# Performance work log

Measured on AMD Instinct MI355X. Metric: run time of the kernel, lower is better.

Reference implementation:

```python
import jax, jax.numpy as jnp
import numpy as np

N = 100_000   # nodes
E = 1_600_000 # edges per edge type
DIN = 128     # input_dim
DH = 128      # prot_hidden_dim
L = 3         # prot_num_layers
EPS = 1e-5


def setup_inputs() -> dict:
    key = jax.random.key(0)
    ks = jax.random.split(key, 8)
    s = 1.0 / np.sqrt(DH)
    return {
        "x": jax.random.normal(ks[0], (N, DIN), jnp.float32),
        "src": jax.random.randint(ks[1], (3, E), 0, N, jnp.int32),
        "dst": jax.random.randint(ks[2], (3, E), 0, N, jnp.int32),
        "gc_W0": jax.random.normal(ks[3], (3, DIN, DH), jnp.float32) * s,
        "gc_b0": jnp.zeros((3, DH), jnp.float32),
        "gc_W": jax.random.normal(ks[4], (L - 1, 3, DH, DH), jnp.float32) * s,
        "gc_b": jnp.zeros((L - 1, 3, DH), jnp.float32),
        "fc_W": jax.random.normal(ks[5], (L, DH, DH), jnp.float32) * s,
        "fc_b": jnp.zeros((L, DH), jnp.float32),
        "bn_gamma": jnp.ones((L, DH), jnp.float32),
        "bn_beta": jnp.zeros((L, DH), jnp.float32),
    }


def _graph_conv(x, src, dst, W, b):
    # DGL GraphConv, norm='both': D_in^{-1/2} A D_out^{-1/2} X W + b
    ones = jnp.ones(src.shape[0], x.dtype)
    deg_out = jnp.clip(jax.ops.segment_sum(ones, src, num_segments=N), 1.0)
    deg_in = jnp.clip(jax.ops.segment_sum(ones, dst, num_segments=N), 1.0)
    # apply weight first (same math; keeps gathered message width = DH)
    h = (x * jax.lax.rsqrt(deg_out)[:, None]) @ W  # [N, DH]
    agg = jax.ops.segment_sum(h[src], dst, num_segments=N)  # gather + scatter-add
    return agg * jax.lax.rsqrt(deg_in)[:, None] + b


def _batchnorm(x, gamma, beta):
    # training-mode BatchNorm1d: biased batch statistics
    mu = jnp.mean(x, axis=0)
    var = jnp.mean(jnp.square(x - mu), axis=0)
    return (x - mu) * jax.lax.rsqrt(var + EPS) * gamma + beta


def reference(x, src, dst, gc_W0, gc_b0, gc_W, gc_b, fc_W, fc_b, bn_gamma, bn_beta):
    h = x
    for l in range(L):
        W = gc_W0 if l == 0 else gc_W[l - 1]
        b = gc_b0 if l == 0 else gc_b[l - 1]
        # HeteroGraphConv with aggregate='sum' over 3 edge types
        out = _graph_conv(h, src[0], dst[0], W[0], b[0])
        for e in range(1, 3):
            out = out + _graph_conv(h, src[e], dst[e], W[e], b[e])
        # FC -> ReLU -> BatchNorm (dropout = identity in eval mode)
        h = _batchnorm(jax.nn.relu(out @ fc_W[l] + fc_b[l]), bn_gamma[l], bn_beta[l])
    return h
```

## Files before the change

kernel.cpp:

```cpp
#include <hip/hip_runtime.h>


#define EPSV 1e-5f
#define CH 4096
#define MAXNB 512

typedef _Float16 h2v __attribute__((ext_vector_type(2)));
typedef _Float16 f16x8 __attribute__((ext_vector_type(8)));
typedef __attribute__((ext_vector_type(4))) float f4v;

__global__ void coarse_hist(const int* __restrict__ src, const int* __restrict__ dst,
                            int* __restrict__ chd, int* __restrict__ chs,
                            int E, int NB) {
    __shared__ int hd[MAXNB], hs[MAXNB];
    int t = blockIdx.y;
    for (int i = threadIdx.x; i < MAXNB; i += 256) { hd[i] = 0; hs[i] = 0; }
    __syncthreads();
    int base = blockIdx.x * CH;
    int end = base + CH < E ? base + CH : E;
    const int* sp = src + (size_t)t * E;
    const int* dp = dst + (size_t)t * E;
    for (int i = base + threadIdx.x; i < end; i += 256) {
        atomicAdd(&hd[dp[i] >> 8], 1);
        atomicAdd(&hs[sp[i] >> 8], 1);
    }
    __syncthreads();
    for (int b = threadIdx.x; b < NB; b += 256) {
        if (hd[b]) atomicAdd(&chd[t * NB + b], hd[b]);
        if (hs[b]) atomicAdd(&chs[t * NB + b], hs[b]);
    }
}

__global__ void scan_off(const int* __restrict__ chd, const int* __restrict__ chs,
                         int* __restrict__ offd, int* __restrict__ offs,
                         int* __restrict__ gcd, int* __restrict__ gcs,
                         int* __restrict__ rowptr, int NB, int N, int E) {
    __shared__ int s[MAXNB];
    int tid = threadIdx.x;
    for (int a = 0; a < 6; ++a) {
        const int* h = (a < 3) ? chd + a * NB : chs + (a - 3) * NB;
        int* off = (a < 3) ? offd + a * (NB + 1) : offs + (a - 3) * (NB + 1);
        int* gc = (a < 3) ? gcd + a * NB : gcs + (a - 3) * NB;
        s[tid] = (tid < NB) ? h[tid] : 0;
        __syncthreads();
        for (int o = 1; o < MAXNB; o <<= 1) {
            int v = (tid >= o) ? s[tid - o] : 0;
            __syncthreads();
            s[tid] += v;
            __syncthreads();
        }
        if (tid < NB) {
            off[tid + 1] = s[tid];
            if (tid == 0) off[0] = 0;
        }
        __syncthreads();
        if (tid < NB) gc[tid] = off[tid];
        __syncthreads();
    }
    if (tid < 3) rowptr[tid * (N + 1) + N] = E;
}

__launch_bounds__(256)
__global__ void scatter_coarse(const int* __restrict__ src, const int* __restrict__ dst,
                               int* __restrict__ gcd, int* __restrict__ gcs,
                               int* __restrict__ dbuf, unsigned char* __restrict__ sbuf,
                               int E, int NB) {
    __shared__ int hd[MAXNB], hs[MAXNB];
    __shared__ int lod[MAXNB], los[MAXNB];
    __shared__ int bd[MAXNB], bs[MAXNB];
    __shared__ int rbi[CH];
    __shared__ unsigned char rbs[CH];
    const int tid = threadIdx.x;
    const int t = blockIdx.y;
    const int base = blockIdx.x * CH;
    const int end = base + CH < E ? base + CH : E;
    const int cnt = end - base;
    const int* sp = src + (size_t)t * E;
    const int* dp = dst + (size_t)t * E;

    for (int i = tid; i < MAXNB; i += 256) { hd[i] = 0; hs[i] = 0; }
    __syncthreads();
    for (int i = base + tid; i < end; i += 256) {
        atomicAdd(&hd[dp[i] >> 8], 1);
        atomicAdd(&hs[sp[i] >> 8], 1);
    }
    __syncthreads();
    for (int b = tid; b < NB; b += 256) {
        bd[b] = hd[b] ? atomicAdd(&gcd[t * NB + b], hd[b]) : 0;
        bs[b] = hs[b] ? atomicAdd(&gcs[t * NB + b], hs[b]) : 0;
    }
    lod[tid] = hd[tid]; lod[tid + 256] = hd[tid + 256];
    los[tid] = hs[tid]; los[tid + 256] = hs[tid + 256];
    __syncthreads();
    for (int o = 1; o < MAXNB; o <<= 1) {
        int a0 = lod[tid], a1 = lod[tid + 256];
        int b0 = los[tid], b1 = los[tid + 256];
        int p0 = (tid >= o) ? lod[tid - o] : 0;
        int p1 = lod[tid + 256 - o];
        int q0 = (tid >= o) ? los[tid - o] : 0;
        int q1 = los[tid + 256 - o];
        __syncthreads();
        lod[tid] = a0 + p0; lod[tid + 256] = a1 + p1;
        los[tid] = b0 + q0; los[tid + 256] = b1 + q1;
        __syncthreads();
    }
    hd[tid] = lod[tid] - hd[tid]; hd[tid + 256] = lod[tid + 256] - hd[tid + 256];
    hs[tid] = los[tid] - hs[tid]; hs[tid + 256] = los[tid + 256] - hs[tid + 256];
    __syncthreads();
    for (int i = base + tid; i < end; i += 256) {
        int sv = sp[i], dv = dp[i];
        int lp = atomicAdd(&hd[dv >> 8], 1);
        rbi[lp] = (sv << 8) | (dv & 255);
        int ls = atomicAdd(&hs[sv >> 8], 1);
        rbs[ls] = (unsigned char)(sv & 255);
    }
    __syncthreads();
    for (int i = tid; i < cnt; i += 256) {
        int lo = 0, hi = NB - 1;
        while (lo < hi) { int mid = (lo + hi) >> 1; if (lod[mid] > i) hi = mid; else lo = mid + 1; }
        int excl = lo ? lod[lo - 1] : 0;
        dbuf[(size_t)t * E + bd[lo] + (i - excl)] = rbi[i];
    }
    for (int i = tid; i < cnt; i += 256) {
        int lo = 0, hi = NB - 1;
        while (lo < hi) { int mid = (lo + hi) >> 1; if (los[mid] > i) hi = mid; else lo = mid + 1; }
        int excl = lo ? los[lo - 1] : 0;
        sbuf[(size_t)t * E + bs[lo] + (i - excl)] = rbs[i];
    }
}

__global__ void fine_src(const unsigned char* __restrict__ sbuf, const int* __restrict__ offs,
                         float* __restrict__ dro, int E, int N, int NB) {
    __shared__ int h[256];
    int b = blockIdx.x, t = blockIdx.y;
    int tid = threadIdx.x;
    h[tid] = 0;
    __syncthreads();
    int beg = offs[t * (NB + 1) + b], end = offs[t * (NB + 1) + b + 1];
    const unsigned char* sp = sbuf + (size_t)t * E;
    for (int i = beg + tid; i < end; i += 256) atomicAdd(&h[sp[i]], 1);
    __syncthreads();
    int node = b * 256 + tid;
    if (node < N) {
        int dg = h[tid] < 1 ? 1 : h[tid];
        dro[(size_t)t * N + node] = rsqrtf((float)dg);
    }
}

#define FDCAP 6656
__global__ void fine_dst(const int* __restrict__ dbuf, const int* __restrict__ offd,
                         const float* __restrict__ dro, int* __restrict__ erec,
                         int* __restrict__ rowptr, float* __restrict__ dri,
                         int E, int N, int NB) {
    __shared__ int h[256], sc[256], cur[256];
    __shared__ int rb[FDCAP];
    int b = blockIdx.x, t = blockIdx.y;
    int tid = threadIdx.x;
    h[tid] = 0;
    __syncthreads();
    int beg = offd[t * (NB + 1) + b], end = offd[t * (NB + 1) + b + 1];
    int cnt = end - beg;
    const int* dp = dbuf + (size_t)t * E;
    const float* drt = dro + (size_t)t * N;
    for (int i = beg + tid; i < end; i += 256) atomicAdd(&h[dp[i] & 255], 1);
    __syncthreads();
    sc[tid] = h[tid];
    __syncthreads();
    for (int o = 1; o < 256; o <<= 1) {
        int v = (tid >= o) ? sc[tid - o] : 0;
        __syncthreads();
        sc[tid] += v;
        __syncthreads();
    }
    int excl = sc[tid] - h[tid];
    cur[tid] = excl;
    int node = b * 256 + tid;
    if (node < N) {
        rowptr[t * (N + 1) + node] = beg + excl;
        int dg = h[tid] < 1 ? 1 : h[tid];
        dri[(size_t)t * N + node] = rsqrtf((float)dg);
    }
    __syncthreads();
    if (cnt <= FDCAP) {
        for (int i = beg + tid; i < end; i += 256) {
            int v = dp[i];
            int p = atomicAdd(&cur[v & 255], 1);
            rb[p] = v >> 8;
        }
        __syncthreads();
        for (int i = tid; i < cnt; i += 256) {
            int sv = rb[i];
            int wq = (int)(drt[sv] * 4095.0f + 0.5f);
            erec[(size_t)t * E + beg + i] = sv | (wq << 20);
        }
    } else {
        for (int i = beg + tid; i < end; i += 256) {
            int v = dp[i];
            int sv = v >> 8;
            int wq = (int)(drt[sv] * 4095.0f + 0.5f);
            int p = beg + atomicAdd(&cur[v & 255], 1);
            erec[(size_t)t * E + p] = sv | (wq << 20);
        }
    }
}

__device__ __forceinline__ h2v ash2(unsigned u) {
    union { unsigned u; h2v h; } c;
    c.u = u;
    return c.h;
}
__device__ __forceinline__ unsigned packh2(float lo, float hi) {
    union { h2v h; unsigned u; } c;
    c.h = (h2v){(_Float16)lo, (_Float16)hi};
    return c.u;
}
__device__ __forceinline__ unsigned short f16b(float f) {
    union { _Float16 h; unsigned short s; } c;
    c.h = (_Float16)f;
    return c.s;
}

__global__ void cvt_f16(const float* __restrict__ h, unsigned short* __restrict__ h2,
                        int total8) {
    int i = blockIdx.x * 256 + threadIdx.x;
    if (i >= total8) return;
    const float4* hp = (const float4*)h + (size_t)i * 2;
    float4 v0 = hp[0], v1 = hp[1];
    uint4 o;
    o.x = packh2(v0.x, v0.y);
    o.y = packh2(v0.z, v0.w);
    o.z = packh2(v1.x, v1.y);
    o.w = packh2(v1.z, v1.w);
    ((uint4*)h2)[i] = o;
}

__global__ void pack_w(const float* __restrict__ gcW0, const float* __restrict__ gcW,
                       const float* __restrict__ fcW, unsigned short* __restrict__ Wg,
                       unsigned short* __restrict__ Wf) {
    int mat = blockIdx.x;
    const float* srcp;
    unsigned short* dstp;
    if (mat < 9) {
        int l = mat / 3, e = mat % 3;
        srcp = (l == 0) ? gcW0 + (size_t)e * 16384
                        : gcW + ((size_t)(l - 1) * 3 + e) * 16384;
        dstp = Wg + (size_t)mat * 16384;
    } else {
        srcp = fcW + (size_t)(mat - 9) * 16384;
        dstp = Wf + (size_t)(mat - 9) * 16384;
    }
    for (int p = threadIdx.x; p < 16384; p += 256) {
        int j = p & 7;
        int ln = (p >> 3) & 63;
        int nt = (p >> 9) & 7;
        int ks = p >> 12;
        int k = ks * 32 + (ln >> 4) * 8 + j;
        int n = nt * 16 + (ln & 15);
        dstp[p] = f16b(srcp[k * 128 + n]);
    }
}

template <int AFF>
__launch_bounds__(256)
__global__ void agg_kernel(const unsigned short* __restrict__ h2, const int* __restrict__ rowptrB,
                           const int* __restrict__ erecB, const float* __restrict__ driB,
                           const float* __restrict__ bnsum, const float* __restrict__ gamma,
                           const float* __restrict__ beta, float invn,
                           unsigned short* __restrict__ zB, int N, int E) {
    __shared__ float lss[256];
    if (AFF) {
        int tid = threadIdx.x;
        if (tid < 128) {
            float mean = bnsum[tid] * invn;
            float var = bnsum[128 + tid] * invn - mean * mean;
            float sc = gamma[tid] * rsqrtf(var + EPSV);
            lss[tid] = sc;
            lss[128 + tid] = beta[tid] - mean * sc;
        }
        __syncthreads();
    }
    const int e = blockIdx.y;
    const int* rowptr = rowptrB + e * (N + 1);
    const int* erec = erecB + (size_t)e * E;
    const float* dri = driB + (size_t)e * N;
    unsigned short* z = zB + (size_t)e * N * 128;

    int idx = blockIdx.x * 256 + threadIdx.x;
    int node = idx >> 4;
    int lq = idx & 15;
    if (node >= N) return;
    int beg = rowptr[node], end = rowptr[node + 1];
    const uint4* hp = (const uint4*)h2 + lq;
    h2v ac0 = (h2v)0, ac1 = (h2v)0, ac2 = (h2v)0, ac3 = (h2v)0;
    float wacc = 0.f;
    const float IW = 1.0f / 4095.0f;

    int j = beg;
    for (; j + 8 <= end; j += 8) {
        int r[8];
#pragma unroll
        for (int q = 0; q < 8; ++q) r[q] = erec[j + q];
        uint4 u[8];
#pragma unroll
        for (int q = 0; q < 8; ++q) u[q] = hp[(size_t)(r[q] & 0xFFFFF) * 16];
#pragma unroll
        for (int q = 0; q < 8; ++q) {
            float wf = (float)((unsigned)r[q] >> 20) * IW;
            if (AFF) wacc += wf;
            _Float16 wh = (_Float16)wf;
            h2v wp = (h2v){wh, wh};
            ac0 = ash2(u[q].x) * wp + ac0;
            ac1 = ash2(u[q].y) * wp + ac1;
            ac2 = ash2(u[q].z) * wp + ac2;
            ac3 = ash2(u[q].w) * wp + ac3;
        }
    }
    for (; j + 4 <= end; j += 4) {
        int r[4];
#pragma unroll
        for (int q = 0; q < 4; ++q) r[q] = erec[j + q];
        uint4 u[4];
#pragma unroll
        for (int q = 0; q < 4; ++q) u[q] = hp[(size_t)(r[q] & 0xFFFFF) * 16];
#pragma unroll
        for (int q = 0; q < 4; ++q) {
            float wf = (float)((unsigned)r[q] >> 20) * IW;
            if (AFF) wacc += wf;
            _Float16 wh = (_Float16)wf;
            h2v wp = (h2v){wh, wh};
            ac0 = ash2(u[q].x) * wp + ac0;
            ac1 = ash2(u[q].y) * wp + ac1;
            ac2 = ash2(u[q].z) * wp + ac2;
            ac3 = ash2(u[q].w) * wp + ac3;
        }
    }
    for (; j < end; ++j) {
        int r0 = erec[j];
        float wf = (float)((unsigned)r0 >> 20) * IW;
        if (AFF) wacc += wf;
        _Float16 wh = (_Float16)wf;
        h2v wp = (h2v){wh, wh};
        uint4 u0 = hp[(size_t)(r0 & 0xFFFFF) * 16];
        ac0 = ash2(u0.x) * wp + ac0;
        ac1 = ash2(u0.y) * wp + ac1;
        ac2 = ash2(u0.z) * wp + ac2;
        ac3 = ash2(u0.w) * wp + ac3;
    }
    float a0 = (float)ac0[0], a1 = (float)ac0[1];
    float a2 = (float)ac1[0], a3 = (float)ac1[1];
    float a4 = (float)ac2[0], a5 = (float)ac2[1];
    float a6 = (float)ac3[0], a7 = (float)ac3[1];
    float scl = dri[node];
    if (AFF) {
        const float* ap = &lss[lq * 8];
        const float* bp = &lss[128 + lq * 8];
        a0 = ap[0] * a0 + bp[0] * wacc;
        a1 = ap[1] * a1 + bp[1] * wacc;
        a2 = ap[2] * a2 + bp[2] * wacc;
        a3 = ap[3] * a3 + bp[3] * wacc;
        a4 = ap[4] * a4 + bp[4] * wacc;
        a5 = ap[5] * a5 + bp[5] * wacc;
        a6 = ap[6] * a6 + bp[6] * wacc;
        a7 = ap[7] * a7 + bp[7] * wacc;
    }
    uint4 o;
    o.x = packh2(a0 * scl, a1 * scl);
    o.y = packh2(a2 * scl, a3 * scl);
    o.z = packh2(a4 * scl, a5 * scl);
    o.w = packh2(a6 * scl, a7 * scl);
    ((uint4*)z)[(size_t)node * 16 + lq] = o;
}

template <int MODE>
__launch_bounds__(512)
__global__ void mfma_layer(const unsigned short* __restrict__ zB,
                           const unsigned short* __restrict__ Wgp,
                           const float* __restrict__ b3,
                           const unsigned short* __restrict__ Wfp,
                           const float* __restrict__ fcb,
                           unsigned short* __restrict__ outb, float* __restrict__ outf,
                           float* __restrict__ bnsum, int M) {
    __shared__ unsigned short T[128 * 128];
    __shared__ float red[256];
    const int tid = threadIdx.x;
    const int l = tid & 63;
    const int wv = tid >> 6;
    const int wm = wv >> 1;
    const int wn = wv & 1;
    const int m0 = blockIdx.x * 128;
    const int lr = l & 15;
    const int lk = (l >> 4) * 8;

    int rowb[2];
#pragma unroll
    for (int mt = 0; mt < 2; ++mt) {
        int r = m0 + wm * 32 + mt * 16 + lr;
        rowb[mt] = (r < M) ? r : (M - 1);
    }

    {
        f4v acc[2][4];
#pragma unroll
        for (int i = 0; i < 2; ++i)
#pragma unroll
            for (int j = 0; j < 4; ++j) acc[i][j] = (f4v){0.f, 0.f, 0.f, 0.f};
#pragma unroll
        for (int e = 0; e < 3; ++e) {
            const unsigned short* zp = zB + (size_t)e * M * 128;
            const unsigned short* wp = Wgp + (size_t)e * 16384;
#pragma unroll
            for (int ks = 0; ks < 4; ++ks) {
                f16x8 a[2], b[4];
#pragma unroll
                for (int mt = 0; mt < 2; ++mt)
                    a[mt] = *(const f16x8*)(zp + (size_t)rowb[mt] * 128 + ks * 32 + lk);
#pragma unroll
                for (int nt = 0; nt < 4; ++nt)
                    b[nt] = *(const f16x8*)(wp + ks * 4096 + (wn * 4 + nt) * 512 + l * 8);
#pragma unroll
                for (int mt = 0; mt < 2; ++mt)
#pragma unroll
                    for (int nt = 0; nt < 4; ++nt)
                        acc[mt][nt] = __builtin_amdgcn_mfma_f32_16x16x32_f16(
                            a[mt], b[nt], acc[mt][nt], 0, 0, 0);
            }
        }
        float bs[4];
        int col[4];
#pragma unroll
        for (int nt = 0; nt < 4; ++nt) {
            col[nt] = wn * 64 + nt * 16 + lr;
            bs[nt] = b3[col[nt]] + b3[128 + col[nt]] + b3[256 + col[nt]];
        }
#pragma unroll
        for (int mt = 0; mt < 2; ++mt) {
#pragma unroll
            for (int r = 0; r < 4; ++r) {
                int rl = wm * 32 + mt * 16 + (l >> 4) * 4 + r;
#pragma unroll
                for (int nt = 0; nt < 4; ++nt) {
                    int c = col[nt];
                    int chunk = (c >> 3) ^ (rl & 15);
                    T[rl * 128 + chunk * 8 + (c & 7)] = f16b(acc[mt][nt][r] + bs[nt]);
                }
            }
        }
    }
    __syncthreads();

    f4v acc2[2][4];
#pragma unroll
    for (int i = 0; i < 2; ++i)
#pragma unroll
        for (int j = 0; j < 4; ++j) acc2[i][j] = (f4v){0.f, 0.f, 0.f, 0.f};
#pragma unroll
    for (int ks = 0; ks < 4; ++ks) {
        f16x8 a[2], b[4];
#pragma unroll
        for (int mt = 0; mt < 2; ++mt) {
            int rl = wm * 32 + mt * 16 + lr;
            int chunk = (ks * 4 + (l >> 4)) ^ lr;
            a[mt] = *(const f16x8*)&T[rl * 128 + chunk * 8];
        }
#pragma unroll
        for (int nt = 0; nt < 4; ++nt)
            b[nt] = *(const f16x8*)(Wfp + ks * 4096 + (wn * 4 + nt) * 512 + l * 8);
#pragma unroll
        for (int mt = 0; mt < 2; ++mt)
#pragma unroll
            for (int nt = 0; nt < 4; ++nt)
                acc2[mt][nt] = __builtin_amdgcn_mfma_f32_16x16x32_f16(
                    a[mt], b[nt], acc2[mt][nt], 0, 0, 0);
    }

    float bv[4], cs[4] = {}, cq[4] = {};
    int col[4];
#pragma unroll
    for (int nt = 0; nt < 4; ++nt) {
        col[nt] = wn * 64 + nt * 16 + lr;
        bv[nt] = fcb[col[nt]];
    }
#pragma unroll
    for (int mt = 0; mt < 2; ++mt) {
#pragma unroll
        for (int r = 0; r < 4; ++r) {
            int row = m0 + wm * 32 + mt * 16 + (l >> 4) * 4 + r;
            if (row < M) {
#pragma unroll
                for (int nt = 0; nt < 4; ++nt) {
                    float v = acc2[mt][nt][r] + bv[nt];
                    v = v > 0.f ? v : 0.f;
                    cs[nt] += v;
                    cq[nt] += v * v;
                    if (MODE == 0)
                        outb[(size_t)row * 128 + col[nt]] = f16b(v);
                    else
                        outf[(size_t)row * 128 + col[nt]] = v;
                }
            }
        }
    }
    if (tid < 256) red[tid] = 0.f;
    __syncthreads();
#pragma unroll
    for (int nt = 0; nt < 4; ++nt) {
        atomicAdd(&red[col[nt]], cs[nt]);
        atomicAdd(&red[128 + col[nt]], cq[nt]);
    }
    __syncthreads();
    if (tid < 128) {
        atomicAdd(&bnsum[tid], red[tid]);
        atomicAdd(&bnsum[128 + tid], red[128 + tid]);
    }
}

__global__ void bn_apply(float* __restrict__ h, const float* __restrict__ bnsum,
                         const float* __restrict__ gamma, const float* __restrict__ beta,
                         float invn, int total4) {
    __shared__ float lss[256];
    int tid = threadIdx.x;
    if (tid < 128) {
        float mean = bnsum[tid] * invn;
        float var = bnsum[128 + tid] * invn - mean * mean;
        float sc = gamma[tid] * rsqrtf(var + EPSV);
        lss[tid] = sc;
        lss[128 + tid] = beta[tid] - mean * sc;
    }
    __syncthreads();
    int i = blockIdx.x * 256 + tid;
    if (i >= total4) return;
    int c4 = (i & 31) * 4;
    float4 sc = *(const float4*)&lss[c4];
    float4 sh = *(const float4*)&lss[128 + c4];
    float4 v = ((float4*)h)[i];
    v.x = v.x * sc.x + sh.x;
    v.y = v.y * sc.y + sh.y;
    v.z = v.z * sc.z + sh.z;
    v.w = v.w * sc.w + sh.w;
    ((float4*)h)[i] = v;
}

extern "C" void kernel_launch(void* const* d_in, const int* in_sizes, int n_in,
                              void* d_out, int out_size, void* d_ws, size_t ws_size,
                              hipStream_t stream) {
    const float* x    = (const float*)d_in[0];
    const int*   src  = (const int*)d_in[1];
    const int*   dst  = (const int*)d_in[2];
    const float* gcW0 = (const float*)d_in[3];
    const float* gcb0 = (const float*)d_in[4];
    const float* gcW  = (const float*)d_in[5];
    const float* gcb  = (const float*)d_in[6];
    const float* fcW  = (const float*)d_in[7];
    const float* fcb  = (const float*)d_in[8];
    const float* bng  = (const float*)d_in[9];
    const float* bnb  = (const float*)d_in[10];
    float* out = (float*)d_out;

    const int N = in_sizes[0] / 128;
    const int E = in_sizes[1] / 3;
    const int NB = (N + 255) / 256;

    char* w = (char*)d_ws;
    auto alloc = [&](size_t bytes) -> char* {
        char* p = w;
        w += (bytes + 255) & ~(size_t)255;
        return p;
    };
    unsigned short* zB    = (unsigned short*)alloc((size_t)3 * N * 128 * 2);
    unsigned short* h2    = (unsigned short*)alloc((size_t)N * 128 * 2);
    unsigned short* Wg    = (unsigned short*)alloc((size_t)9 * 16384 * 2);
    unsigned short* Wf    = (unsigned short*)alloc((size_t)3 * 16384 * 2);
    int*   erec   = (int*)alloc((size_t)3 * E * 4);
    int*   rowptr = (int*)alloc((size_t)3 * (N + 1) * 4);
    float* dro    = (float*)alloc((size_t)3 * N * 4);
    float* dri    = (float*)alloc((size_t)3 * N * 4);
    int*   chd    = (int*)alloc((size_t)3 * NB * 4);
    int*   chs    = (int*)alloc((size_t)3 * NB * 4);
    int*   offd   = (int*)alloc((size_t)3 * (NB + 1) * 4);
    int*   offs   = (int*)alloc((size_t)3 * (NB + 1) * 4);
    int*   gcd    = (int*)alloc((size_t)3 * NB * 4);
    int*   gcs    = (int*)alloc((size_t)3 * NB * 4);
    float* bnsum  = (float*)alloc(256 * 4);
    int* dbuf = (int*)zB;
    unsigned char* sbuf = (unsigned char*)(dbuf + (size_t)3 * E);

    hipMemsetAsync(chd, 0, (size_t)3 * NB * 4, stream);
    hipMemsetAsync(chs, 0, (size_t)3 * NB * 4, stream);
    dim3 cg2((E + CH - 1) / CH, 3);
    coarse_hist<<<cg2, 256, 0, stream>>>(src, dst, chd, chs, E, NB);
    scan_off<<<1, MAXNB, 0, stream>>>(chd, chs, offd, offs, gcd, gcs, rowptr, NB, N, E);
    scatter_coarse<<<cg2, 256, 0, stream>>>(src, dst, gcd, gcs, dbuf, sbuf, E, NB);
    dim3 fg(NB, 3);
    fine_src<<<fg, 256, 0, stream>>>(sbuf, offs, dro, E, N, NB);
    fine_dst<<<fg, 256, 0, stream>>>(dbuf, offd, dro, erec, rowptr, dri, E, N, NB);

    pack_w<<<12, 256, 0, stream>>>(gcW0, gcW, fcW, Wg, Wf);
    const int cvtGrid = (N * 16 + 255) / 256;
    cvt_f16<<<cvtGrid, 256, 0, stream>>>(x, h2, N * 16);

    const int gemmGrid = (N + 127) / 128;
    const float invn = 1.0f / (float)N;
    dim3 aggG((N * 16 + 255) / 256, 3);

    for (int l = 0; l < 3; ++l) {
        const float* bl = (l == 0) ? gcb0 : gcb + (size_t)(l - 1) * 3 * 128;
        if (l == 0)
            agg_kernel<0><<<aggG, 256, 0, stream>>>(h2, rowptr, erec, dri,
                                                    nullptr, nullptr, nullptr, invn,
                                                    zB, N, E);
        else
            agg_kernel<1><<<aggG, 256, 0, stream>>>(h2, rowptr, erec, dri,
                                                    bnsum, bng + (size_t)(l - 1) * 128,
                                                    bnb + (size_t)(l - 1) * 128, invn,
                                                    zB, N, E);
        hipMemsetAsync(bnsum, 0, 256 * 4, stream);
        if (l < 2)
            mfma_layer<0><<<gemmGrid, 512, 0, stream>>>(zB, Wg + (size_t)l * 3 * 16384, bl,
                                                        Wf + (size_t)l * 16384,
                                                        fcb + (size_t)l * 128,
                                                        h2, nullptr, bnsum, N);
        else
            mfma_layer<1><<<gemmGrid, 512, 0, stream>>>(zB, Wg + (size_t)l * 3 * 16384, bl,
                                                        Wf + (size_t)l * 16384,
                                                        fcb + (size_t)l * 128,
                                                        nullptr, out, bnsum, N);
    }
    bn_apply<<<(N * 32 + 255) / 256, 256, 0, stream>>>(out, bnsum, bng + 2 * 128,
                                                       bnb + 2 * 128, invn, N * 32);
}
```

Measured before the change: 899.8 us.

## Replace global atomic bucket offsets with per-block histograms and deterministic block scan

Coarse histogram now writes per-block bucket counts to global memory, and a new blk_scan kernel computes per-block exclusive prefixes and totals. The scatter pass reads these precomputed offsets instead of re-histogramming its chunk and doing global atomicAdd on bucket cursors. This removes the duplicate histogram pass and the global atomics, and makes the edge order deterministic. In exchange it adds a kernel whose serial per-thread scan over about 391 blocks uses only about 1200 threads with strided, uncoalesced access, plus extra workspace traffic.

```diff
diff --git a/kernel.cpp b/kernel.cpp
--- a/kernel.cpp
+++ b/kernel.cpp
@@ -10,13 +10,14 @@
 typedef __attribute__((ext_vector_type(4))) float f4v;
 
 __global__ void coarse_hist(const int* __restrict__ src, const int* __restrict__ dst,
-                            int* __restrict__ chd, int* __restrict__ chs,
-                            int E, int NB) {
+                            int* __restrict__ bhd, int* __restrict__ bhs,
+                            int E, int NB, int nblk) {
     __shared__ int hd[MAXNB], hs[MAXNB];
-    int t = blockIdx.y;
+    const int t = blockIdx.y;
+    const int blk = blockIdx.x;
     for (int i = threadIdx.x; i < MAXNB; i += 256) { hd[i] = 0; hs[i] = 0; }
     __syncthreads();
-    int base = blockIdx.x * CH;
+    int base = blk * CH;
     int end = base + CH < E ? base + CH : E;
     const int* sp = src + (size_t)t * E;
     const int* dp = dst + (size_t)t * E;
@@ -26,21 +27,42 @@
     }
     __syncthreads();
     for (int b = threadIdx.x; b < NB; b += 256) {
-        if (hd[b]) atomicAdd(&chd[t * NB + b], hd[b]);
-        if (hs[b]) atomicAdd(&chs[t * NB + b], hs[b]);
-    }
+        size_t o = (size_t)(t * NB + b) * nblk + blk;
+        bhd[o] = hd[b];
+        bhs[o] = hs[b];
+    }
+}
+
+__global__ void blk_scan(const int* __restrict__ bhd, const int* __restrict__ bhs,
+                         int* __restrict__ bpd, int* __restrict__ bps,
+                         int* __restrict__ chd, int* __restrict__ chs,
+                         int NB, int nblk) {
+    int id = blockIdx.x * 256 + threadIdx.x;
+    int half = 3 * NB;
+    if (id >= 2 * half) return;
+    bool isS = id >= half;
+    int r = isS ? id - half : id;
+    const int* cnt = isS ? bhs : bhd;
+    int* pfx = isS ? bps : bpd;
+    int* tot = isS ? chs : chd;
+    size_t base = (size_t)r * nblk;
+    int run = 0;
+    for (int b = 0; b < nblk; ++b) {
+        int v = cnt[base + b];
+        pfx[base + b] = run;
+        run += v;
+    }
+    tot[r] = run;
 }
 
 __global__ void scan_off(const int* __restrict__ chd, const int* __restrict__ chs,
                          int* __restrict__ offd, int* __restrict__ offs,
-                         int* __restrict__ gcd, int* __restrict__ gcs,
                          int* __restrict__ rowptr, int NB, int N, int E) {
     __shared__ int s[MAXNB];
     int tid = threadIdx.x;
     for (int a = 0; a < 6; ++a) {
         const int* h = (a < 3) ? chd + a * NB : chs + (a - 3) * NB;
         int* off = (a < 3) ? offd + a * (NB + 1) : offs + (a - 3) * (NB + 1);
-        int* gc = (a < 3) ? gcd + a * NB : gcs + (a - 3) * NB;
         s[tid] = (tid < NB) ? h[tid] : 0;
         __syncthreads();
         for (int o = 1; o < MAXNB; o <<= 1) {
@@ -54,17 +76,17 @@
             if (tid == 0) off[0] = 0;
         }
         __syncthreads();
-        if (tid < NB) gc[tid] = off[tid];
-        __syncthreads();
     }
     if (tid < 3) rowptr[tid * (N + 1) + N] = E;
 }
 
 __launch_bounds__(256)
 __global__ void scatter_coarse(const int* __restrict__ src, const int* __restrict__ dst,
-                               int* __restrict__ gcd, int* __restrict__ gcs,
+                               const int* __restrict__ bhd, const int* __restrict__ bhs,
+                               const int* __restrict__ bpd, const int* __restrict__ bps,
+                               const int* __restrict__ offd, const int* __restrict__ offs,
                                int* __restrict__ dbuf, unsigned char* __restrict__ sbuf,
-                               int E, int NB) {
+                               int E, int NB, int nblk) {
     __shared__ int hd[MAXNB], hs[MAXNB];
     __shared__ int lod[MAXNB], los[MAXNB];
     __shared__ int bd[MAXNB], bs[MAXNB];
@@ -72,22 +94,25 @@
     __shared__ unsigned char rbs[CH];
     const int tid = threadIdx.x;
     const int t = blockIdx.y;
-    const int base = blockIdx.x * CH;
+    const int blk = blockIdx.x;
+    const int base = blk * CH;
     const int end = base + CH < E ? base + CH : E;
     const int cnt = end - base;
     const int* sp = src + (size_t)t * E;
     const int* dp = dst + (size_t)t * E;
 
-    for (int i = tid; i < MAXNB; i += 256) { hd[i] = 0; hs[i] = 0; }
-    __syncthreads();
-    for (int i = base + tid; i < end; i += 256) {
-        atomicAdd(&hd[dp[i] >> 8], 1);
-        atomicAdd(&hs[sp[i] >> 8], 1);
-    }
-    __syncthreads();
-    for (int b = tid; b < NB; b += 256) {
-        bd[b] = hd[b] ? atomicAdd(&gcd[t * NB + b], hd[b]) : 0;
-        bs[b] = hs[b] ? atomicAdd(&gcs[t * NB + b], hs[b]) : 0;
+    for (int b = tid; b < MAXNB; b += 256) {
+        if (b < NB) {
+            size_t o = (size_t)(t * NB + b) * nblk + blk;
+            int cd = bhd[o], cs2 = bhs[o];
+            hd[b] = cd;
+            hs[b] = cs2;
+            bd[b] = offd[t * (NB + 1) + b] + bpd[o];
+            bs[b] = offs[t * (NB + 1) + b] + bps[o];
+        } else {
+            hd[b] = 0;
+            hs[b] = 0;
+        }
     }
     lod[tid] = hd[tid]; lod[tid + 256] = hd[tid + 256];
     los[tid] = hs[tid]; los[tid + 256] = hs[tid + 256];
@@ -559,6 +584,7 @@
     const int N = in_sizes[0] / 128;
     const int E = in_sizes[1] / 3;
     const int NB = (N + 255) / 256;
+    const int nblk = (E + CH - 1) / CH;
 
     char* w = (char*)d_ws;
     auto alloc = [&](size_t bytes) -> char* {
@@ -574,22 +600,24 @@
     int*   rowptr = (int*)alloc((size_t)3 * (N + 1) * 4);
     float* dro    = (float*)alloc((size_t)3 * N * 4);
     float* dri    = (float*)alloc((size_t)3 * N * 4);
+    int*   bhd    = (int*)alloc((size_t)3 * NB * nblk * 4);
+    int*   bhs    = (int*)alloc((size_t)3 * NB * nblk * 4);
+    int*   bpd    = (int*)alloc((size_t)3 * NB * nblk * 4);
+    int*   bps    = (int*)alloc((size_t)3 * NB * nblk * 4);
     int*   chd    = (int*)alloc((size_t)3 * NB * 4);
     int*   chs    = (int*)alloc((size_t)3 * NB * 4);
     int*   offd   = (int*)alloc((size_t)3 * (NB + 1) * 4);
     int*   offs   = (int*)alloc((size_t)3 * (NB + 1) * 4);
-    int*   gcd    = (int*)alloc((size_t)3 * NB * 4);
-    int*   gcs    = (int*)alloc((size_t)3 * NB * 4);
     float* bnsum  = (float*)alloc(256 * 4);
     int* dbuf = (int*)zB;
     unsigned char* sbuf = (unsigned char*)(dbuf + (size_t)3 * E);
 
-    hipMemsetAsync(chd, 0, (size_t)3 * NB * 4, stream);
-    hipMemsetAsync(chs, 0, (size_t)3 * NB * 4, stream);
-    dim3 cg2((E + CH - 1) / CH, 3);
-    coarse_hist<<<cg2, 256, 0, stream>>>(src, dst, chd, chs, E, NB);
-    scan_off<<<1, MAXNB, 0, stream>>>(chd, chs, offd, offs, gcd, gcs, rowptr, NB, N, E);
-    scatter_coarse<<<cg2, 256, 0, stream>>>(src, dst, gcd, gcs, dbuf, sbuf, E, NB);
+    dim3 cg2(nblk, 3);
+    coarse_hist<<<cg2, 256, 0, stream>>>(src, dst, bhd, bhs, E, NB, nblk);
+    blk_scan<<<(2 * 3 * NB + 255) / 256, 256, 0, stream>>>(bhd, bhs, bpd, bps, chd, chs, NB, nblk);
+    scan_off<<<1, MAXNB, 0, stream>>>(chd, chs, offd, offs, rowptr, NB, N, E);
+    scatter_coarse<<<cg2, 256, 0, stream>>>(src, dst, bhd, bhs, bpd, bps, offd, offs,
+                                            dbuf, sbuf, E, NB, nblk);
     dim3 fg(NB, 3);
     fine_src<<<fg, 256, 0, stream>>>(sbuf, offs, dro, E, N, NB);
     fine_dst<<<fg, 256, 0, stream>>>(dbuf, offd, dro, erec, rowptr, dri, E, N, NB);
```

Result: slower. 1.057 ms (+17.4%).
